# Performance work log

Measured on AMD Instinct MI355X. Metric: run time of the kernel, lower is better.

Reference implementation:

```python
import jax, jax.numpy as jnp
import numpy as np
from jax import lax

EPS = 1e-5
NUM_HEADS = 8


def _safe_norm(x):
    # sqrt(max(sum x^2, EPS^2)) == max(||x||, EPS); grad-safe at 0
    return jnp.sqrt(jnp.maximum(jnp.sum(x * x, axis=-1, keepdims=True), EPS * EPS))


def _project(x):
    norm = _safe_norm(x)
    max_norm = 1.0 - EPS
    scale = jnp.where(norm >= max_norm, max_norm / (norm + EPS), jnp.ones_like(norm))
    return x * scale


def _logmap0(y):
    # logarithmic_map(0, y): lambda_0 = 2/(1+EPS)
    y = _project(y)
    n = _safe_norm(y)  # clamp(min=EPS) is built in
    lam = 2.0 / (1.0 + EPS)
    return (2.0 / lam) * jnp.arctanh(n) * (y / n)


def _expmap0(v):
    # exponential_map(0, v): lambda_0 = 2/(1+EPS)
    n = _safe_norm(v)
    lam = 2.0 / (1.0 + EPS)
    return _project(jnp.tanh(lam * n / 2.0) * (v / n))


def _mobius_add(x, y):
    x = _project(x)
    y = _project(y)
    xy = jnp.sum(x * y, axis=-1, keepdims=True)
    xn = jnp.sum(x * x, axis=-1, keepdims=True)
    yn = jnp.sum(y * y, axis=-1, keepdims=True)
    num = (1.0 + 2.0 * xy + yn) * x + (1.0 - xn) * y
    den = 1.0 + 2.0 * xy + xn * yn + EPS
    return _project(num / den)


def _hyp_linear(x, W, b):
    # HyperbolicLinear.forward: project -> logmap0 -> linear -> expmap0 -> mobius-add bias
    x = _project(x)
    xt = _logmap0(x)
    t = xt @ W.T
    r = _expmap0(t)
    r = _mobius_add(r, jnp.broadcast_to(b, r.shape))
    return r


def setup_inputs() -> dict:
    key = jax.random.key(0)
    ks = jax.random.split(key, 11)
    B, S, E = 4, 512, 512

    def xavier(k, shape):
        bound = np.sqrt(6.0 / (shape[0] + shape[1]))
        return jax.random.uniform(k, shape, jnp.float32, -bound, bound)

    return {
        "query": jax.random.normal(ks[0], (B, S, E), jnp.float32),
        "key": jax.random.normal(ks[1], (B, S, E), jnp.float32),
        "value": jax.random.normal(ks[2], (B, S, E), jnp.float32),
        "Wq": xavier(ks[3], (E, E)), "bq": 0.01 * jax.random.normal(ks[4], (E,), jnp.float32),
        "Wk": xavier(ks[5], (E, E)), "bk": 0.01 * jax.random.normal(ks[6], (E,), jnp.float32),
        "Wv": xavier(ks[7], (E, E)), "bv": 0.01 * jax.random.normal(ks[8], (E,), jnp.float32),
        "Wo": xavier(ks[9], (E, E)), "bo": 0.01 * jax.random.normal(ks[10], (E,), jnp.float32),
    }


def reference(query, key, value, Wq, bq, Wk, bk, Wv, bv, Wo, bo):
    B, S, E = query.shape
    H = NUM_HEADS
    D = E // H

    Q = _hyp_linear(query, Wq, bq).reshape(B, S, H, D).transpose(0, 2, 1, 3)  # [B,H,S,D]
    K = _hyp_linear(key, Wk, bk).reshape(B, S, H, D).transpose(0, 2, 1, 3)
    V = _hyp_linear(value, Wv, bv).reshape(B, S, H, D).transpose(0, 2, 1, 3)

    # Pairwise Poincare distance: d(q,k) = acosh(1 + 2||q-k||^2/((1-|q|^2)(1-|k|^2)) + EPS)
    q = _project(Q)
    k = _project(K)
    qn = jnp.sum(q * q, axis=-1)  # [B,H,S]
    kn = jnp.sum(k * k, axis=-1)  # [B,H,S]
    qk = jnp.einsum('bhqd,bhkd->bhqk', q, k)
    num = jnp.maximum(qn[..., :, None] + kn[..., None, :] - 2.0 * qk, 0.0)
    den = jnp.maximum((1.0 - qn)[..., :, None] * (1.0 - kn)[..., None, :], EPS)
    dist = jnp.arccosh(1.0 + 2.0 * num / den + EPS)  # [B,H,Sq,Sk]
    attn = jax.nn.softmax(-dist, axis=-1)

    # Sequential Mobius-add accumulation over key/value positions
    wt = jnp.moveaxis(attn, 3, 0)  # [Sk,B,H,Sq]
    vt = jnp.moveaxis(V, 2, 0)     # [Sk,B,H,D]

    @jax.checkpoint
    def step(ws, wv):
        wj, vj = wv  # wj: [B,H,Sq], vj: [B,H,D]
        return _mobius_add(ws, wj[..., None] * vj[:, :, None, :]), None

    ws0 = jnp.zeros((B, H, S, D), query.dtype)
    attended, _ = lax.scan(step, ws0, (wt, vt))  # [B,H,Sq,D]

    attended = attended.transpose(0, 2, 1, 3).reshape(B, S, E)
    return _hyp_linear(attended, Wo, bo)
```

## Files before the change

kernel.cpp:

```cpp
#include <hip/hip_runtime.h>
#include <math.h>

#define EPS  1e-5f
#define EPS2 1e-10f
#define MAXN (1.0f - EPS)

using short8  = __attribute__((ext_vector_type(8))) short;
using floatx4 = __attribute__((ext_vector_type(4))) float;
using float2v = __attribute__((ext_vector_type(2))) float;

template <int CTRL>
static __device__ __forceinline__ float qperm(float x) {
  return __int_as_float(__builtin_amdgcn_update_dpp(
      __float_as_int(x), __float_as_int(x), CTRL, 0xF, 0xF, false));
}
#define QP_XOR1    0xB1
#define QP_XOR2    0x4E
#define QP_HALFMIR 0x141

#if __has_builtin(__builtin_elementwise_fma)
static __device__ __forceinline__ float2v fma2(float2v a, float2v b, float2v c) {
  return __builtin_elementwise_fma(a, b, c);
}
#else
static __device__ __forceinline__ float2v fma2(float2v a, float2v b, float2v c) {
  float2v r; r.x = fmaf(a.x, b.x, c.x); r.y = fmaf(a.y, b.y, c.y); return r;
}
#endif

static __device__ __forceinline__ int pack_hi2(float a, float b) {
  return (int)((__float_as_uint(a) >> 16) | (__float_as_uint(b) & 0xFFFF0000u));
}
static __device__ __forceinline__ float hi_of(float a) {
  return __uint_as_float(__float_as_uint(a) & 0xFFFF0000u);
}

static __device__ __forceinline__ float logmap_f(float ss) {
  const float r = sqrtf(fmaxf(ss, EPS2));
  float at;
  if (r >= MAXN) {
    at = 0.5f * logf((r * (2.0f - EPS) + EPS) / (EPS * (1.0f + r)));
  } else {
    at = 0.5f * logf((1.0f + r) / (1.0f - r));
  }
  return (1.0f + EPS) * at / r;
}

__global__ __launch_bounds__(256) void k_gemm_mfma(
    const float* __restrict__ A0, const float* __restrict__ A1, const float* __restrict__ A2,
    const float* __restrict__ W0, const float* __restrict__ W1, const float* __restrict__ W2,
    float* __restrict__ Cbase) {
  const int z = blockIdx.z;
  const float* A = (z == 0) ? A0 : ((z == 1) ? A1 : A2);
  const float* W = (z == 0) ? W0 : ((z == 1) ? W1 : W2);
  float* C = Cbase + (size_t)z * (2048 * 512);
  __shared__ int Ahi[64][36], Alo[64][36], Whi[64][36], Wlo[64][36];
  __shared__ float f_lds[64];
  const int t = threadIdx.x;
  const int n0 = blockIdx.x * 64;
  const int m0 = blockIdx.y * 64;
  const int row = t >> 2, c0 = (t & 3) * 16, ci = (t & 3) * 8;
  const int w = t >> 6, lane = t & 63;
  const int quad = lane >> 4, l16 = lane & 15;
  const int mw = (w & 1) * 32, nw = (w >> 1) * 32;
  floatx4 acc[2][2];
#pragma unroll
  for (int i = 0; i < 2; ++i)
#pragma unroll
    for (int j = 0; j < 2; ++j) acc[i][j] = (floatx4){0.f, 0.f, 0.f, 0.f};
  float ssq = 0.0f;

  for (int k0 = 0; k0 < 512; k0 += 64) {
    float4 av[4], wv[4];
#pragma unroll
    for (int i = 0; i < 4; ++i) {
      av[i] = *(const float4*)&A[(size_t)(n0 + row) * 512 + k0 + c0 + 4 * i];
      wv[i] = *(const float4*)&W[(size_t)(m0 + row) * 512 + k0 + c0 + 4 * i];
    }
    int pAh[8], pAl[8], pWh[8], pWl[8];
#pragma unroll
    for (int i = 0; i < 4; ++i) {
      ssq = fmaf(av[i].x, av[i].x, ssq); ssq = fmaf(av[i].y, av[i].y, ssq);
      ssq = fmaf(av[i].z, av[i].z, ssq); ssq = fmaf(av[i].w, av[i].w, ssq);
      pAh[2 * i]     = pack_hi2(av[i].x, av[i].y);
      pAh[2 * i + 1] = pack_hi2(av[i].z, av[i].w);
      pAl[2 * i]     = pack_hi2(av[i].x - hi_of(av[i].x), av[i].y - hi_of(av[i].y));
      pAl[2 * i + 1] = pack_hi2(av[i].z - hi_of(av[i].z), av[i].w - hi_of(av[i].w));
      pWh[2 * i]     = pack_hi2(wv[i].x, wv[i].y);
      pWh[2 * i + 1] = pack_hi2(wv[i].z, wv[i].w);
      pWl[2 * i]     = pack_hi2(wv[i].x - hi_of(wv[i].x), wv[i].y - hi_of(wv[i].y));
      pWl[2 * i + 1] = pack_hi2(wv[i].z - hi_of(wv[i].z), wv[i].w - hi_of(wv[i].w));
    }
    __syncthreads();
    *(int4*)&Ahi[row][ci]     = *(int4*)&pAh[0];
    *(int4*)&Ahi[row][ci + 4] = *(int4*)&pAh[4];
    *(int4*)&Alo[row][ci]     = *(int4*)&pAl[0];
    *(int4*)&Alo[row][ci + 4] = *(int4*)&pAl[4];
    *(int4*)&Whi[row][ci]     = *(int4*)&pWh[0];
    *(int4*)&Whi[row][ci + 4] = *(int4*)&pWh[4];
    *(int4*)&Wlo[row][ci]     = *(int4*)&pWl[0];
    *(int4*)&Wlo[row][ci + 4] = *(int4*)&pWl[4];
    __syncthreads();
#pragma unroll
    for (int kk = 0; kk < 64; kk += 32) {
      short8 ah[2], al[2], bh[2], bl[2];
#pragma unroll
      for (int i = 0; i < 2; ++i) {
        ah[i] = *(const short8*)&((const short*)Ahi[mw + i * 16 + l16])[kk + quad * 8];
        al[i] = *(const short8*)&((const short*)Alo[mw + i * 16 + l16])[kk + quad * 8];
        bh[i] = *(const short8*)&((const short*)Whi[nw + i * 16 + l16])[kk + quad * 8];
        bl[i] = *(const short8*)&((const short*)Wlo[nw + i * 16 + l16])[kk + quad * 8];
      }
#pragma unroll
      for (int i = 0; i < 2; ++i)
#pragma unroll
        for (int j = 0; j < 2; ++j) {
          acc[i][j] = __builtin_amdgcn_mfma_f32_16x16x32_bf16(ah[i], bh[j], acc[i][j], 0, 0, 0);
          acc[i][j] = __builtin_amdgcn_mfma_f32_16x16x32_bf16(ah[i], bl[j], acc[i][j], 0, 0, 0);
          acc[i][j] = __builtin_amdgcn_mfma_f32_16x16x32_bf16(al[i], bh[j], acc[i][j], 0, 0, 0);
        }
    }
  }
  ssq += qperm<QP_XOR1>(ssq);
  ssq += qperm<QP_XOR2>(ssq);
  if ((t & 3) == 0) f_lds[row] = logmap_f(ssq);
  __syncthreads();
#pragma unroll
  for (int i = 0; i < 2; ++i) {
    const int lrow_base = mw + i * 16 + quad * 4;
#pragma unroll
    for (int r = 0; r < 4; ++r) {
      const float fv = f_lds[lrow_base + r];
#pragma unroll
      for (int j = 0; j < 2; ++j)
        C[(size_t)(n0 + lrow_base + r) * 512 + m0 + nw + j * 16 + l16] = fv * acc[i][j][r];
    }
  }
}

__global__ __launch_bounds__(256) void k_post(const float* __restrict__ tin,
                                              const float* __restrict__ b0,
                                              const float* __restrict__ b1,
                                              const float* __restrict__ b2,
                                              float* __restrict__ o0, float* __restrict__ o1,
                                              float* __restrict__ o2,
                                              float* __restrict__ nrm0, float* __restrict__ nrm1,
                                              float* __restrict__ nrm2,
                                              float* __restrict__ rowsum_init, int final_mode) {
  const int nrow = blockIdx.x, z = blockIdx.y, t = threadIdx.x;
  const float* tv = tin + ((size_t)z * 2048 + nrow) * 512;
  const float* bias = (z == 0) ? b0 : ((z == 1) ? b1 : b2);
  const int e0 = 2 * t;
  const float2 tp = *(const float2*)&tv[e0];
  const float2 bp = *(const float2*)&bias[e0];
  float p_tt = tp.x * tp.x + tp.y * tp.y;
  float p_tb = tp.x * bp.x + tp.y * bp.y;
  float p_bb = bp.x * bp.x + bp.y * bp.y;
#pragma unroll
  for (int m = 32; m; m >>= 1) {
    p_tt += __shfl_xor(p_tt, m, 64);
    p_tb += __shfl_xor(p_tb, m, 64);
    p_bb += __shfl_xor(p_bb, m, 64);
  }
  __shared__ float red[4][3];
  const int lane = t & 63, w = t >> 6;
  if (lane == 0) { red[w][0] = p_tt; red[w][1] = p_tb; red[w][2] = p_bb; }
  __syncthreads();
  const float s_tt = red[0][0] + red[1][0] + red[2][0] + red[3][0];
  const float s_tb = red[0][1] + red[1][1] + red[2][1] + red[3][1];
  const float s_bb = red[0][2] + red[1][2] + red[2][2] + red[3][2];
  const float tn = sqrtf(fmaxf(s_tt, EPS2));
  const float th = tanhf(tn / (1.0f + EPS));
  const float g = th / tn;
  const float rnorm = th * (sqrtf(s_tt) / tn);
  const float sr = (rnorm >= MAXN) ? (MAXN / (rnorm + EPS)) : 1.0f;
  const float gr = g * sr;
  const float rn = (rnorm * sr) * (rnorm * sr);
  const float bnorm = sqrtf(fmaxf(s_bb, EPS2));
  const float sb = (bnorm >= MAXN) ? (MAXN / (bnorm + EPS)) : 1.0f;
  const float xy = gr * sb * s_tb;
  const float yn = (sb * sb) * s_bb;
  const float Af = 1.0f + 2.0f * xy + yn;
  const float Cf = 1.0f - rn;
  const float den = 1.0f + 2.0f * xy + rn * yn + EPS;
  const float id = 1.0f / den;
  const float on_raw = (Af * Af * rn + 2.0f * Af * Cf * xy + Cf * Cf * yn) * (id * id);
  const float no = sqrtf(fmaxf(on_raw, EPS2));
  const float so = (no >= MAXN) ? (MAXN / (no + EPS)) : 1.0f;
  const float ms = id * so;
  const float ca = gr * Af * ms;
  const float cb = sb * Cf * ms;
  const float v0 = ca * tp.x + cb * bp.x;
  const float v1 = ca * tp.y + cb * bp.y;
  if (final_mode) {
    float2 o; o.x = v0; o.y = v1;
    *(float2*)&o0[(size_t)nrow * 512 + e0] = o;
    return;
  }
  float hp = v0 * v0 + v1 * v1;
#pragma unroll
  for (int m = 16; m; m >>= 1) hp += __shfl_xor(hp, m, 64);
  const float hnr = sqrtf(fmaxf(hp, EPS2));
  float sh = 1.0f;
  if (z != 2) sh = (hnr >= MAXN) ? (MAXN / (hnr + EPS)) : 1.0f;
  float* outz = (z == 0) ? o0 : ((z == 1) ? o1 : o2);
  float* nz = (z == 0) ? nrm0 : ((z == 1) ? nrm1 : nrm2);
  const int b = nrow >> 9, s = nrow & 511, h = e0 >> 6, d = e0 & 63;
  float2 o; o.x = v0 * sh; o.y = v1 * sh;
  *(float2*)&outz[(((size_t)(b * 8 + h) * 512 + s) * 64 + d)] = o;
  if ((t & 31) == 0) nz[(size_t)(b * 8 + h) * 512 + s] = hp * sh * sh;
  if (z == 0 && t < 8) rowsum_init[((size_t)(nrow >> 9) * 8 + t) * 512 + (nrow & 511)] = 0.0f;
}

__global__ __launch_bounds__(256) void k_logits(const float* __restrict__ Q,
                                                const float* __restrict__ K,
                                                const float* __restrict__ qn,
                                                const float* __restrict__ kn,
                                                float* __restrict__ attn,
                                                float* __restrict__ rowsum) {
  const int bh = blockIdx.z;
  const int i0 = blockIdx.x * 64;
  const int j0 = blockIdx.y * 64;
  const float* Qb = Q + (size_t)bh * 512 * 64;
  const float* Kb = K + (size_t)bh * 512 * 64;
  __shared__ int Qhi[64][36], Qlo[64][36], Khi[64][36], Klo[64][36];
  const int t = threadIdx.x;
  const int row = t >> 2, c0 = (t & 3) * 16, ci = (t & 3) * 8;
  const int w = t >> 6, lane = t & 63;
  const int quad = lane >> 4, l16 = lane & 15;
  const int mw = (w & 1) * 32, nw = (w >> 1) * 32;
  float4 qv4[4], kv4[4];
#pragma unroll
  for (int i = 0; i < 4; ++i) {
    qv4[i] = *(const float4*)&Qb[(size_t)(i0 + row) * 64 + c0 + 4 * i];
    kv4[i] = *(const float4*)&Kb[(size_t)(j0 + row) * 64 + c0 + 4 * i];
  }
  int pQh[8], pQl[8], pKh[8], pKl[8];
#pragma unroll
  for (int i = 0; i < 4; ++i) {
    pQh[2 * i]     = pack_hi2(qv4[i].x, qv4[i].y);
    pQh[2 * i + 1] = pack_hi2(qv4[i].z, qv4[i].w);
    pQl[2 * i]     = pack_hi2(qv4[i].x - hi_of(qv4[i].x), qv4[i].y - hi_of(qv4[i].y));
    pQl[2 * i + 1] = pack_hi2(qv4[i].z - hi_of(qv4[i].z), qv4[i].w - hi_of(qv4[i].w));
    pKh[2 * i]     = pack_hi2(kv4[i].x, kv4[i].y);
    pKh[2 * i + 1] = pack_hi2(kv4[i].z, kv4[i].w);
    pKl[2 * i]     = pack_hi2(kv4[i].x - hi_of(kv4[i].x), kv4[i].y - hi_of(kv4[i].y));
    pKl[2 * i + 1] = pack_hi2(kv4[i].z - hi_of(kv4[i].z), kv4[i].w - hi_of(kv4[i].w));
  }
  *(int4*)&Qhi[row][ci]     = *(int4*)&pQh[0];
  *(int4*)&Qhi[row][ci + 4] = *(int4*)&pQh[4];
  *(int4*)&Qlo[row][ci]     = *(int4*)&pQl[0];
  *(int4*)&Qlo[row][ci + 4] = *(int4*)&pQl[4];
  *(int4*)&Khi[row][ci]     = *(int4*)&pKh[0];
  *(int4*)&Khi[row][ci + 4] = *(int4*)&pKh[4];
  *(int4*)&Klo[row][ci]     = *(int4*)&pKl[0];
  *(int4*)&Klo[row][ci + 4] = *(int4*)&pKl[4];
  __syncthreads();
  floatx4 acc[2][2];
#pragma unroll
  for (int i = 0; i < 2; ++i)
#pragma unroll
    for (int j = 0; j < 2; ++j) acc[i][j] = (floatx4){0.f, 0.f, 0.f, 0.f};
#pragma unroll
  for (int kk = 0; kk < 64; kk += 32) {
    short8 ah[2], al[2], bhv[2], blv[2];
#pragma unroll
    for (int i = 0; i < 2; ++i) {
      ah[i]  = *(const short8*)&((const short*)Qhi[mw + i * 16 + l16])[kk + quad * 8];
      al[i]  = *(const short8*)&((const short*)Qlo[mw + i * 16 + l16])[kk + quad * 8];
      bhv[i] = *(const short8*)&((const short*)Khi[nw + i * 16 + l16])[kk + quad * 8];
      blv[i] = *(const short8*)&((const short*)Klo[nw + i * 16 + l16])[kk + quad * 8];
    }
#pragma unroll
    for (int i = 0; i < 2; ++i)
#pragma unroll
      for (int j = 0; j < 2; ++j) {
        acc[i][j] = __builtin_amdgcn_mfma_f32_16x16x32_bf16(ah[i], bhv[j], acc[i][j], 0, 0, 0);
        acc[i][j] = __builtin_amdgcn_mfma_f32_16x16x32_bf16(ah[i], blv[j], acc[i][j], 0, 0, 0);
        acc[i][j] = __builtin_amdgcn_mfma_f32_16x16x32_bf16(al[i], bhv[j], acc[i][j], 0, 0, 0);
      }
  }
#pragma unroll
  for (int i = 0; i < 2; ++i) {
    float rs_acc[4] = {0.f, 0.f, 0.f, 0.f};
#pragma unroll
    for (int r = 0; r < 4; ++r) {
      const int grow = i0 + mw + i * 16 + quad * 4 + r;
      const float qni = qn[(size_t)bh * 512 + grow];
      const float rq = 1.0f - qni;
#pragma unroll
      for (int j = 0; j < 2; ++j) {
        const int gcol = j0 + nw + j * 16 + l16;
        const float knj = kn[(size_t)bh * 512 + gcol];
        const float num = fmaxf(qni + knj - 2.0f * acc[i][j][r], 0.0f);
        const float den = fmaxf(rq * (1.0f - knj), EPS);
        const float wv = fmaf(2.0f * num, __builtin_amdgcn_rcpf(den), EPS);
        const float s_ = 1.0f + wv + sqrtf(wv * (wv + 2.0f));
        const float rr = __builtin_amdgcn_rcpf(s_);
        rs_acc[r] += rr;
        attn[((size_t)bh * 512 + grow) * 512 + gcol] = rr;
      }
    }
#pragma unroll
    for (int r = 0; r < 4; ++r) {
      float v = rs_acc[r];
      v += __shfl_xor(v, 1, 64); v += __shfl_xor(v, 2, 64);
      v += __shfl_xor(v, 4, 64); v += __shfl_xor(v, 8, 64);
      if (l16 == 0)
        atomicAdd(&rowsum[(size_t)bh * 512 + i0 + mw + i * 16 + quad * 4 + r], v);
    }
  }
}

__global__ __launch_bounds__(256) void k_scan(const float* __restrict__ V,
                                              const float* __restrict__ vn,
                                              const float* __restrict__ rw,
                                              const float* __restrict__ rowsum,
                                              float* __restrict__ att) {
  __shared__ __align__(16) float v_lds[64 * 64];
  __shared__ __align__(16) float swyn_lds[64 * 66];
  const int blk = blockIdx.x;
  const int bh = blk >> 4;
  const int i0 = (blk & 15) * 32;
  const int t = threadIdx.x;
  const int lane = t & 63, w = t >> 6;
  const int row_blk = w * 8 + (lane >> 3);
  const int sub = lane & 7;
  const int d0 = sub * 8;
  const float* Vb = V + (size_t)bh * 512 * 64;
  const float* vnb = vn + (size_t)bh * 512;
  const float* arow = rw + ((size_t)bh * 512 + i0 + row_blk) * 512;
  const float inv_s = __builtin_amdgcn_rcpf(rowsum[(size_t)bh * 512 + i0 + row_blk]);

  float2v wsv[4];
#pragma unroll
  for (int k = 0; k < 4; ++k) wsv[k] = (float2v){0.f, 0.f};
  float xn = 0.0f;

  for (int jc = 0; jc < 512; jc += 64) {
#pragma unroll
    for (int it = 0; it < 4; ++it) {
      const int idx4 = it * 256 + t;
      *(float4*)&v_lds[idx4 * 4] = *(const float4*)&Vb[(size_t)jc * 64 + idx4 * 4];
    }
    const float4 a0 = *(const float4*)&arow[jc + sub * 8];
    const float4 a1 = *(const float4*)&arow[jc + sub * 8 + 4];
    const float4 n0 = *(const float4*)&vnb[jc + sub * 8];
    const float4 n1 = *(const float4*)&vnb[jc + sub * 8 + 4];
    const float wq[8] = {a0.x, a0.y, a0.z, a0.w, a1.x, a1.y, a1.z, a1.w};
    const float nq[8] = {n0.x, n0.y, n0.z, n0.w, n1.x, n1.y, n1.z, n1.w};
#pragma unroll
    for (int e = 0; e < 8; ++e) {
      const float wgt = wq[e] * inv_s;
      float2 p; p.x = wgt; p.y = (wgt * wgt) * nq[e];
      *(float2*)&swyn_lds[(sub * 8 + e) * 66 + row_blk * 2] = p;
    }
    __syncthreads();

#pragma unroll
    for (int j = 0; j < 64; ++j) {
      const float2 sy2 = *(const float2*)&swyn_lds[j * 66 + row_blk * 2];
      const float4 v0 = *(const float4*)&v_lds[j * 64 + d0];
      const float4 v1 = *(const float4*)&v_lds[j * 64 + d0 + 4];
      const float2v vv0 = {v0.x, v0.y}, vv1 = {v0.z, v0.w};
      const float2v vv2 = {v1.x, v1.y}, vv3 = {v1.z, v1.w};
      const float sw = sy2.x, yn = sy2.y;
      const float xnyn1 = fmaf(xn, yn, 1.0f + EPS);
      const float sxy   = xn + yn;
      const float ynp1  = 1.0f + yn;
      const float Cfsw  = (1.0f - xn) * sw;
      float2v da = wsv[0] * vv0;
      da = fma2(wsv[1], vv1, da);
      float2v db = wsv[2] * vv2;
      db = fma2(wsv[3], vv3, db);
      const float2v sv = da + db;
      float d = sv.x + sv.y;
      d += qperm<QP_XOR1>(d);
      d += qperm<QP_XOR2>(d);
      d += qperm<QP_HALFMIR>(d);
      const float xy  = sw * d;
      const float den = fmaf(2.0f, xy, xnyn1);
      const float s2  = fmaf(2.0f, xy, sxy);
      const float Af  = fmaf(2.0f, xy, ynp1);
      const float id  = __builtin_amdgcn_rcpf(den);
      const float dn  = den - EPS;
      const float am  = Af * id;
      const float cm  = Cfsw * id;
      xn = (s2 * id) * (dn * id);
      const float2v amv = {am, am};
      const float2v cmv = {cm, cm};
      wsv[0] = fma2(amv, wsv[0], cmv * vv0);
      wsv[1] = fma2(amv, wsv[1], cmv * vv1);
      wsv[2] = fma2(amv, wsv[2], cmv * vv2);
      wsv[3] = fma2(amv, wsv[3], cmv * vv3);
    }
    __syncthreads();
  }
  const int b = bh >> 3, h = bh & 7;
  float* o = att + (((size_t)b * 512 + i0 + row_blk) * 512 + h * 64 + d0);
  float4 s0; s0.x = wsv[0].x; s0.y = wsv[0].y; s0.z = wsv[1].x; s0.w = wsv[1].y;
  float4 s1; s1.x = wsv[2].x; s1.y = wsv[2].y; s1.z = wsv[3].x; s1.w = wsv[3].y;
  *(float4*)&o[0] = s0;
  *(float4*)&o[4] = s1;
}

extern "C" void kernel_launch(void* const* d_in, const int* in_sizes, int n_in,
                              void* d_out, int out_size, void* d_ws, size_t ws_size,
                              hipStream_t stream) {
  const float* query = (const float*)d_in[0];
  const float* key_  = (const float*)d_in[1];
  const float* value = (const float*)d_in[2];
  const float* Wq = (const float*)d_in[3];
  const float* bq = (const float*)d_in[4];
  const float* Wk = (const float*)d_in[5];
  const float* bk = (const float*)d_in[6];
  const float* Wv = (const float*)d_in[7];
  const float* bv = (const float*)d_in[8];
  const float* Wo = (const float*)d_in[9];
  const float* bo = (const float*)d_in[10];
  float* ws = (float*)d_ws;
  const size_t M = 1u << 20;
  float* Qb     = ws;
  float* Kb     = ws + 1 * M;
  float* Vb     = ws + 2 * M;
  float* qn     = ws + 3 * M;
  float* kn     = qn + 16384;
  float* vn     = kn + 16384;
  float* rowsum = vn + 16384;
  float* rw     = ws + 4 * M;
  float* t3     = ws + 12 * M;
  float* att    = ws + 15 * M;
  float* to_    = ws + 16 * M;

  k_gemm_mfma<<<dim3(32, 8, 3), 256, 0, stream>>>(query, key_, value, Wq, Wk, Wv, t3);
  k_post<<<dim3(2048, 3), 256, 0, stream>>>(t3, bq, bk, bv, Qb, Kb, Vb, qn, kn, vn,
                                            rowsum, 0);
  k_logits<<<dim3(8, 8, 32), 256, 0, stream>>>(Qb, Kb, qn, kn, rw, rowsum);
  k_scan<<<512, 256, 0, stream>>>(Vb, vn, rw, rowsum, att);
  k_gemm_mfma<<<dim3(32, 8, 1), 256, 0, stream>>>(att, att, att, Wo, Wo, Wo, to_);
  k_post<<<dim3(2048, 1), 256, 0, stream>>>(to_, bo, bo, bo, (float*)d_out,
                                            nullptr, nullptr, nullptr, nullptr, nullptr,
                                            nullptr, 1);
}
```

Before: 229.8 us.

## Unroll Mobius scan two steps at a time using precomputed adjacent V dot products

The sequential Mobius-add scan now processes key positions in pairs. Both dot products of the running state with V[j] and V[j+1] are computed against the same old state, and the second is corrected algebraically using a precomputed g_j = V[j]·V[j+1] stored in LDS. Two steps are folded into one state update, cutting the length of the serial dependency chain on the cross-lane reductions and the LDS traffic per step. In exchange it adds a per-block prologue that reads V to compute the pair dot products, more registers, and a slightly different floating-point rounding order.

```diff
diff --git a/kernel.cpp b/kernel.cpp
--- a/kernel.cpp
+++ b/kernel.cpp
@@ -318,7 +318,8 @@
                                               const float* __restrict__ rowsum,
                                               float* __restrict__ att) {
   __shared__ __align__(16) float v_lds[64 * 64];
-  __shared__ __align__(16) float swyn_lds[64 * 66];
+  __shared__ __align__(16) float sy_lds[32][132];
+  __shared__ __align__(16) float g_lds[256];
   const int blk = blockIdx.x;
   const int bh = blk >> 4;
   const int i0 = (blk & 15) * 32;
@@ -332,6 +333,19 @@
   const float* arow = rw + ((size_t)bh * 512 + i0 + row_blk) * 512;
   const float inv_s = __builtin_amdgcn_rcpf(rowsum[(size_t)bh * 512 + i0 + row_blk]);
 
+  {
+    const float* vp = Vb + (size_t)(2 * t) * 64;
+    float acc = 0.0f;
+#pragma unroll
+    for (int i = 0; i < 16; ++i) {
+      const float4 x = *(const float4*)&vp[4 * i];
+      const float4 y = *(const float4*)&vp[64 + 4 * i];
+      acc = fmaf(x.x, y.x, acc); acc = fmaf(x.y, y.y, acc);
+      acc = fmaf(x.z, y.z, acc); acc = fmaf(x.w, y.w, acc);
+    }
+    g_lds[t] = acc;
+  }
+
   float2v wsv[4];
 #pragma unroll
   for (int k = 0; k < 4; ++k) wsv[k] = (float2v){0.f, 0.f};
@@ -350,49 +364,65 @@
     const float wq[8] = {a0.x, a0.y, a0.z, a0.w, a1.x, a1.y, a1.z, a1.w};
     const float nq[8] = {n0.x, n0.y, n0.z, n0.w, n1.x, n1.y, n1.z, n1.w};
 #pragma unroll
-    for (int e = 0; e < 8; ++e) {
-      const float wgt = wq[e] * inv_s;
-      float2 p; p.x = wgt; p.y = (wgt * wgt) * nq[e];
-      *(float2*)&swyn_lds[(sub * 8 + e) * 66 + row_blk * 2] = p;
+    for (int k = 0; k < 4; ++k) {
+      const float s0 = wq[2 * k] * inv_s;
+      const float s1 = wq[2 * k + 1] * inv_s;
+      float4 pkt;
+      pkt.x = s0; pkt.y = (s0 * s0) * nq[2 * k];
+      pkt.z = s1; pkt.w = (s1 * s1) * nq[2 * k + 1];
+      *(float4*)&sy_lds[row_blk][sub * 16 + 4 * k] = pkt;
     }
     __syncthreads();
 
 #pragma unroll
-    for (int j = 0; j < 64; ++j) {
-      const float2 sy2 = *(const float2*)&swyn_lds[j * 66 + row_blk * 2];
-      const float4 v0 = *(const float4*)&v_lds[j * 64 + d0];
-      const float4 v1 = *(const float4*)&v_lds[j * 64 + d0 + 4];
-      const float2v vv0 = {v0.x, v0.y}, vv1 = {v0.z, v0.w};
-      const float2v vv2 = {v1.x, v1.y}, vv3 = {v1.z, v1.w};
-      const float sw = sy2.x, yn = sy2.y;
-      const float xnyn1 = fmaf(xn, yn, 1.0f + EPS);
-      const float sxy   = xn + yn;
-      const float ynp1  = 1.0f + yn;
-      const float Cfsw  = (1.0f - xn) * sw;
-      float2v da = wsv[0] * vv0;
-      da = fma2(wsv[1], vv1, da);
-      float2v db = wsv[2] * vv2;
-      db = fma2(wsv[3], vv3, db);
-      const float2v sv = da + db;
-      float d = sv.x + sv.y;
-      d += qperm<QP_XOR1>(d);
-      d += qperm<QP_XOR2>(d);
-      d += qperm<QP_HALFMIR>(d);
-      const float xy  = sw * d;
-      const float den = fmaf(2.0f, xy, xnyn1);
-      const float s2  = fmaf(2.0f, xy, sxy);
-      const float Af  = fmaf(2.0f, xy, ynp1);
-      const float id  = __builtin_amdgcn_rcpf(den);
-      const float dn  = den - EPS;
-      const float am  = Af * id;
-      const float cm  = Cfsw * id;
-      xn = (s2 * id) * (dn * id);
-      const float2v amv = {am, am};
-      const float2v cmv = {cm, cm};
-      wsv[0] = fma2(amv, wsv[0], cmv * vv0);
-      wsv[1] = fma2(amv, wsv[1], cmv * vv1);
-      wsv[2] = fma2(amv, wsv[2], cmv * vv2);
-      wsv[3] = fma2(amv, wsv[3], cmv * vv3);
+    for (int p = 0; p < 32; ++p) {
+      const int j = 2 * p;
+      const float4 sy4 = *(const float4*)&sy_lds[row_blk][4 * p];
+      const float gj = g_lds[(jc >> 1) + p];
+      const float4 va0 = *(const float4*)&v_lds[j * 64 + d0];
+      const float4 va1 = *(const float4*)&v_lds[j * 64 + d0 + 4];
+      const float4 vb0 = *(const float4*)&v_lds[(j + 1) * 64 + d0];
+      const float4 vb1 = *(const float4*)&v_lds[(j + 1) * 64 + d0 + 4];
+      const float2v a0v = {va0.x, va0.y}, a1v = {va0.z, va0.w};
+      const float2v a2v = {va1.x, va1.y}, a3v = {va1.z, va1.w};
+      const float2v b0v = {vb0.x, vb0.y}, b1v = {vb0.z, vb0.w};
+      const float2v b2v = {vb1.x, vb1.y}, b3v = {vb1.z, vb1.w};
+      float2v pa = wsv[0] * a0v; pa = fma2(wsv[1], a1v, pa);
+      float2v pb = wsv[2] * a2v; pb = fma2(wsv[3], a3v, pb);
+      float2v qa = wsv[0] * b0v; qa = fma2(wsv[1], b1v, qa);
+      float2v qb = wsv[2] * b2v; qb = fma2(wsv[3], b3v, qb);
+      const float2v ps = pa + pb;
+      const float2v qs = qa + qb;
+      float dd = ps.x + ps.y;
+      float ee = qs.x + qs.y;
+      dd += qperm<QP_XOR1>(dd);    ee += qperm<QP_XOR1>(ee);
+      dd += qperm<QP_XOR2>(dd);    ee += qperm<QP_XOR2>(ee);
+      dd += qperm<QP_HALFMIR>(dd); ee += qperm<QP_HALFMIR>(ee);
+      const float sw0 = sy4.x, yn0 = sy4.y;
+      const float xy0  = sw0 * dd;
+      const float den0 = fmaf(2.0f, xy0, fmaf(xn, yn0, 1.0f + EPS));
+      const float s20  = fmaf(2.0f, xy0, xn + yn0);
+      const float Af0  = fmaf(2.0f, xy0, 1.0f + yn0);
+      const float id0  = __builtin_amdgcn_rcpf(den0);
+      const float am0  = Af0 * id0;
+      const float cm0  = ((1.0f - xn) * sw0) * id0;
+      const float xn1  = (s20 * id0) * ((den0 - EPS) * id0);
+      const float sw1 = sy4.z, yn1 = sy4.w;
+      const float dd1  = fmaf(am0, ee, cm0 * gj);
+      const float xy1  = sw1 * dd1;
+      const float den1 = fmaf(2.0f, xy1, fmaf(xn1, yn1, 1.0f + EPS));
+      const float s21  = fmaf(2.0f, xy1, xn1 + yn1);
+      const float Af1  = fmaf(2.0f, xy1, 1.0f + yn1);
+      const float id1  = __builtin_amdgcn_rcpf(den1);
+      const float am1  = Af1 * id1;
+      const float cm1  = ((1.0f - xn1) * sw1) * id1;
+      xn = (s21 * id1) * ((den1 - EPS) * id1);
+      const float A2 = am1 * am0, Bc = am1 * cm0;
+      const float2v A2v = {A2, A2}, Bv = {Bc, Bc}, Cv = {cm1, cm1};
+      wsv[0] = fma2(A2v, wsv[0], fma2(Bv, a0v, Cv * b0v));
+      wsv[1] = fma2(A2v, wsv[1], fma2(Bv, a1v, Cv * b1v));
+      wsv[2] = fma2(A2v, wsv[2], fma2(Bv, a2v, Cv * b2v));
+      wsv[3] = fma2(A2v, wsv[3], fma2(Bv, a3v, Cv * b3v));
     }
     __syncthreads();
   }
```

New measurement: 247.1 us. +7.5%, slower.

## Give each scan thread 16 dims over 4 lanes, 64 rows per block

Applied to the files above, without the earlier changes.

The sequential Mobius scan kernel now assigns 16 feature dimensions per thread with 4 lanes per query row, instead of 8 dims with 8 lanes. Each block covers 64 rows, so the grid is halved to 256 blocks. The per-step cross-lane dot-product reduction drops one DPP stage, and each V tile loaded into LDS is reused across twice as many rows. The weight/norm staging buffer is transposed to a row-major layout written with float4 stores. The trade-off is 256 blocks on a 256-CU GPU, which may leave occupancy and latency hiding low, and more registers per thread.

```diff
diff --git a/kernel.cpp b/kernel.cpp
--- a/kernel.cpp
+++ b/kernel.cpp
@@ -318,23 +318,23 @@
                                               const float* __restrict__ rowsum,
                                               float* __restrict__ att) {
   __shared__ __align__(16) float v_lds[64 * 64];
-  __shared__ __align__(16) float swyn_lds[64 * 66];
+  __shared__ __align__(16) float sy_lds[64 * 132];
   const int blk = blockIdx.x;
-  const int bh = blk >> 4;
-  const int i0 = (blk & 15) * 32;
+  const int bh = blk >> 3;
+  const int i0 = (blk & 7) * 64;
   const int t = threadIdx.x;
   const int lane = t & 63, w = t >> 6;
-  const int row_blk = w * 8 + (lane >> 3);
-  const int sub = lane & 7;
-  const int d0 = sub * 8;
+  const int row_blk = w * 16 + (lane >> 2);
+  const int sub = lane & 3;
+  const int d0 = sub * 16;
   const float* Vb = V + (size_t)bh * 512 * 64;
   const float* vnb = vn + (size_t)bh * 512;
   const float* arow = rw + ((size_t)bh * 512 + i0 + row_blk) * 512;
   const float inv_s = __builtin_amdgcn_rcpf(rowsum[(size_t)bh * 512 + i0 + row_blk]);
 
-  float2v wsv[4];
-#pragma unroll
-  for (int k = 0; k < 4; ++k) wsv[k] = (float2v){0.f, 0.f};
+  float2v wsv[8];
+#pragma unroll
+  for (int k = 0; k < 8; ++k) wsv[k] = (float2v){0.f, 0.f};
   float xn = 0.0f;
 
   for (int jc = 0; jc < 512; jc += 64) {
@@ -343,41 +343,55 @@
       const int idx4 = it * 256 + t;
       *(float4*)&v_lds[idx4 * 4] = *(const float4*)&Vb[(size_t)jc * 64 + idx4 * 4];
     }
-    const float4 a0 = *(const float4*)&arow[jc + sub * 8];
-    const float4 a1 = *(const float4*)&arow[jc + sub * 8 + 4];
-    const float4 n0 = *(const float4*)&vnb[jc + sub * 8];
-    const float4 n1 = *(const float4*)&vnb[jc + sub * 8 + 4];
-    const float wq[8] = {a0.x, a0.y, a0.z, a0.w, a1.x, a1.y, a1.z, a1.w};
-    const float nq[8] = {n0.x, n0.y, n0.z, n0.w, n1.x, n1.y, n1.z, n1.w};
-#pragma unroll
-    for (int e = 0; e < 8; ++e) {
-      const float wgt = wq[e] * inv_s;
-      float2 p; p.x = wgt; p.y = (wgt * wgt) * nq[e];
-      *(float2*)&swyn_lds[(sub * 8 + e) * 66 + row_blk * 2] = p;
+    {
+      const float* ar = arow + jc + sub * 16;
+      const float* nr = vnb + jc + sub * 16;
+#pragma unroll
+      for (int q = 0; q < 2; ++q) {
+        const float4 a0 = *(const float4*)&ar[8 * q];
+        const float4 a1 = *(const float4*)&ar[8 * q + 4];
+        const float4 nn0 = *(const float4*)&nr[8 * q];
+        const float4 nn1 = *(const float4*)&nr[8 * q + 4];
+        const float s0 = a0.x * inv_s, s1 = a0.y * inv_s, s2 = a0.z * inv_s, s3 = a0.w * inv_s;
+        const float s4 = a1.x * inv_s, s5 = a1.y * inv_s, s6 = a1.z * inv_s, s7 = a1.w * inv_s;
+        float4 p0, p1, p2, p3;
+        p0.x = s0; p0.y = (s0 * s0) * nn0.x; p0.z = s1; p0.w = (s1 * s1) * nn0.y;
+        p1.x = s2; p1.y = (s2 * s2) * nn0.z; p1.z = s3; p1.w = (s3 * s3) * nn0.w;
+        p2.x = s4; p2.y = (s4 * s4) * nn1.x; p2.z = s5; p2.w = (s5 * s5) * nn1.y;
+        p3.x = s6; p3.y = (s6 * s6) * nn1.z; p3.z = s7; p3.w = (s7 * s7) * nn1.w;
+        const int base = row_blk * 132 + 2 * (sub * 16 + 8 * q);
+        *(float4*)&sy_lds[base]      = p0;
+        *(float4*)&sy_lds[base + 4]  = p1;
+        *(float4*)&sy_lds[base + 8]  = p2;
+        *(float4*)&sy_lds[base + 12] = p3;
+      }
     }
     __syncthreads();
 
 #pragma unroll
     for (int j = 0; j < 64; ++j) {
-      const float2 sy2 = *(const float2*)&swyn_lds[j * 66 + row_blk * 2];
-      const float4 v0 = *(const float4*)&v_lds[j * 64 + d0];
-      const float4 v1 = *(const float4*)&v_lds[j * 64 + d0 + 4];
-      const float2v vv0 = {v0.x, v0.y}, vv1 = {v0.z, v0.w};
-      const float2v vv2 = {v1.x, v1.y}, vv3 = {v1.z, v1.w};
+      const float2 sy2 = *(const float2*)&sy_lds[row_blk * 132 + 2 * j];
+      const float4 u0 = *(const float4*)&v_lds[j * 64 + d0];
+      const float4 u1 = *(const float4*)&v_lds[j * 64 + d0 + 4];
+      const float4 u2 = *(const float4*)&v_lds[j * 64 + d0 + 8];
+      const float4 u3 = *(const float4*)&v_lds[j * 64 + d0 + 12];
+      const float2v vv0 = {u0.x, u0.y}, vv1 = {u0.z, u0.w};
+      const float2v vv2 = {u1.x, u1.y}, vv3 = {u1.z, u1.w};
+      const float2v vv4 = {u2.x, u2.y}, vv5 = {u2.z, u2.w};
+      const float2v vv6 = {u3.x, u3.y}, vv7 = {u3.z, u3.w};
       const float sw = sy2.x, yn = sy2.y;
       const float xnyn1 = fmaf(xn, yn, 1.0f + EPS);
       const float sxy   = xn + yn;
       const float ynp1  = 1.0f + yn;
       const float Cfsw  = (1.0f - xn) * sw;
-      float2v da = wsv[0] * vv0;
-      da = fma2(wsv[1], vv1, da);
-      float2v db = wsv[2] * vv2;
-      db = fma2(wsv[3], vv3, db);
-      const float2v sv = da + db;
+      float2v da = wsv[0] * vv0; da = fma2(wsv[1], vv1, da);
+      float2v db = wsv[2] * vv2; db = fma2(wsv[3], vv3, db);
+      float2v dc = wsv[4] * vv4; dc = fma2(wsv[5], vv5, dc);
+      float2v de = wsv[6] * vv6; de = fma2(wsv[7], vv7, de);
+      const float2v sv = (da + db) + (dc + de);
       float d = sv.x + sv.y;
       d += qperm<QP_XOR1>(d);
       d += qperm<QP_XOR2>(d);
-      d += qperm<QP_HALFMIR>(d);
       const float xy  = sw * d;
       const float den = fmaf(2.0f, xy, xnyn1);
       const float s2  = fmaf(2.0f, xy, sxy);
@@ -393,6 +407,10 @@
       wsv[1] = fma2(amv, wsv[1], cmv * vv1);
       wsv[2] = fma2(amv, wsv[2], cmv * vv2);
       wsv[3] = fma2(amv, wsv[3], cmv * vv3);
+      wsv[4] = fma2(amv, wsv[4], cmv * vv4);
+      wsv[5] = fma2(amv, wsv[5], cmv * vv5);
+      wsv[6] = fma2(amv, wsv[6], cmv * vv6);
+      wsv[7] = fma2(amv, wsv[7], cmv * vv7);
     }
     __syncthreads();
   }
@@ -400,8 +418,12 @@
   float* o = att + (((size_t)b * 512 + i0 + row_blk) * 512 + h * 64 + d0);
   float4 s0; s0.x = wsv[0].x; s0.y = wsv[0].y; s0.z = wsv[1].x; s0.w = wsv[1].y;
   float4 s1; s1.x = wsv[2].x; s1.y = wsv[2].y; s1.z = wsv[3].x; s1.w = wsv[3].y;
-  *(float4*)&o[0] = s0;
-  *(float4*)&o[4] = s1;
+  float4 s2; s2.x = wsv[4].x; s2.y = wsv[4].y; s2.z = wsv[5].x; s2.w = wsv[5].y;
+  float4 s3; s3.x = wsv[6].x; s3.y = wsv[6].y; s3.z = wsv[7].x; s3.w = wsv[7].y;
+  *(float4*)&o[0]  = s0;
+  *(float4*)&o[4]  = s1;
+  *(float4*)&o[8]  = s2;
+  *(float4*)&o[12] = s3;
 }
 
 extern "C" void kernel_launch(void* const* d_in, const int* in_sizes, int n_in,
@@ -436,7 +458,7 @@
   k_post<<<dim3(2048, 3), 256, 0, stream>>>(t3, bq, bk, bv, Qb, Kb, Vb, qn, kn, vn,
                                             rowsum, 0);
   k_logits<<<dim3(8, 8, 32), 256, 0, stream>>>(Qb, Kb, qn, kn, rw, rowsum);
-  k_scan<<<512, 256, 0, stream>>>(Vb, vn, rw, rowsum, att);
+  k_scan<<<256, 256, 0, stream>>>(Vb, vn, rw, rowsum, att);
   k_gemm_mfma<<<dim3(32, 8, 1), 256, 0, stream>>>(att, att, att, Wo, Wo, Wo, to_);
   k_post<<<dim3(2048, 1), 256, 0, stream>>>(to_, bo, bo, bo, (float*)d_out,
                                             nullptr, nullptr, nullptr, nullptr, nullptr,
```

Measured after the change: 236.2 us. 1.03x slower.
